# Kernel tuning notes

Hardware: AMD Instinct MI355X
Metric: run time of the kernel (lower is better)

Reference implementation:

```python
import jax, jax.numpy as jnp
import numpy as np

EPS = 1e-6
NUM_HEADS = 16

def _ln(x):
    # LayerNorm32, no affine, eps=1e-6, computed in fp32
    x32 = x.astype(jnp.float32)
    mu = jnp.mean(x32, axis=-1, keepdims=True)
    var = jnp.var(x32, axis=-1, keepdims=True)
    return ((x32 - mu) * jax.lax.rsqrt(var + EPS)).astype(x.dtype)

def _mha(q, k, v):
    # q,k,v: [B, L, H, D]
    d = q.shape[-1]
    scale = 1.0 / jnp.sqrt(jnp.asarray(d, q.dtype))
    s = jnp.einsum('bqhd,bkhd->bhqk', q, k) * scale
    p = jax.nn.softmax(s, axis=-1)
    o = jnp.einsum('bhqk,bkhd->bqhd', p, v)
    return o.reshape(o.shape[0], o.shape[1], -1)

def setup_inputs() -> dict:
    key = jax.random.key(0)
    ks = jax.random.split(key, 10)
    B, L, C, Lc, Cc = 4, 2048, 1024, 1024, 1024
    Dff = 4 * C
    s = 0.02
    return {
        'x': jax.random.normal(ks[0], (B, L, C), jnp.float32),
        'context': jax.random.normal(ks[1], (B, Lc, Cc), jnp.float32),
        'w_qkv': jax.random.normal(ks[2], (C, 3 * C), jnp.float32) * s,
        'b_qkv': jnp.zeros((3 * C,), jnp.float32),
        'w_os': jax.random.normal(ks[3], (C, C), jnp.float32) * s,
        'b_os': jnp.zeros((C,), jnp.float32),
        'w_qc': jax.random.normal(ks[4], (C, C), jnp.float32) * s,
        'b_qc': jnp.zeros((C,), jnp.float32),
        'w_kvc': jax.random.normal(ks[5], (Cc, 2 * C), jnp.float32) * s,
        'b_kvc': jnp.zeros((2 * C,), jnp.float32),
        'w_oc': jax.random.normal(ks[6], (C, C), jnp.float32) * s,
        'b_oc': jnp.zeros((C,), jnp.float32),
        'w_fc1': jax.random.normal(ks[7], (C, Dff), jnp.float32) * s,
        'b_fc1': jnp.zeros((Dff,), jnp.float32),
        'w_fc2': jax.random.normal(ks[8], (Dff, C), jnp.float32) * s,
        'b_fc2': jnp.zeros((C,), jnp.float32),
    }

def reference(x, context, w_qkv, b_qkv, w_os, b_os, w_qc, b_qc, w_kvc, b_kvc,
              w_oc, b_oc, w_fc1, b_fc1, w_fc2, b_fc2):
    B, L, C = x.shape
    H = NUM_HEADS
    D = C // H
    # --- self attention (pre-norm, full) ---
    h = _ln(x)
    qkv = (h @ w_qkv + b_qkv).reshape(B, L, 3, H, D)
    q, k, v = qkv[:, :, 0], qkv[:, :, 1], qkv[:, :, 2]
    h = _mha(q, k, v) @ w_os + b_os
    x = x + h
    # --- cross attention ---
    h = _ln(x)
    q = (h @ w_qc + b_qc).reshape(B, L, H, D)
    Lc = context.shape[1]
    kv = (context @ w_kvc + b_kvc).reshape(B, Lc, 2, H, D)
    k, v = kv[:, :, 0], kv[:, :, 1]
    h = _mha(q, k, v) @ w_oc + b_oc
    x = x + h
    # --- sparse FFN (GELU tanh) ---
    h = _ln(x)
    h = jax.nn.gelu(h @ w_fc1 + b_fc1, approximate=True) @ w_fc2 + b_fc2
    return x + h
```

## Files before the change

### kernel.cpp

```cpp
#include <hip/hip_runtime.h>

typedef unsigned short ushort_t;
typedef __attribute__((ext_vector_type(8))) short short8;
typedef __attribute__((ext_vector_type(4))) float f32x4;
typedef __attribute__((ext_vector_type(4))) unsigned short ushort4v;

__device__ inline ushort_t f2bf(float f) {
    union { float f; unsigned u; } v; v.f = f;
    return (ushort_t)((v.u + 0x7FFFu + ((v.u >> 16) & 1u)) >> 16);
}
__device__ inline float bf2f(ushort_t u) {
    union { unsigned u; float f; } v; v.u = ((unsigned)u) << 16;
    return v.f;
}

__device__ inline void gld16(const ushort_t* g, ushort_t* l) {
    __builtin_amdgcn_global_load_lds(
        (const __attribute__((address_space(1))) unsigned int*)g,
        (__attribute__((address_space(3))) unsigned int*)l, 16, 0, 0);
}

__device__ inline int xcd_swz(int id, int nwg) {
    int q = nwg >> 3;
    return (id & 7) * q + (id >> 3);
}

__global__ void w_transpose_bf16(const float* __restrict__ w, ushort_t* __restrict__ out,
                                 int K, int N) {
    __shared__ float t[64][65];
    const int k0 = blockIdx.y * 64, n0 = blockIdx.x * 64;
    const int tid = threadIdx.x;
#pragma unroll
    for (int i = 0; i < 16; i++) {
        int idx = tid + i * 256;
        int r = idx >> 6, c = idx & 63;
        t[r][c] = w[(size_t)(k0 + r) * N + n0 + c];
    }
    __syncthreads();
#pragma unroll
    for (int i = 0; i < 16; i++) {
        int idx = tid + i * 256;
        int nr = idx >> 6, kc = idx & 63;
        out[(size_t)(n0 + nr) * K + k0 + kc] = f2bf(t[kc][nr]);
    }
}

__global__ void v_transpose(const ushort_t* __restrict__ V, int vStride, int rowsPerBatch,
                            ushort_t* __restrict__ Vt, int Lk) {
    __shared__ __align__(16) ushort_t t[64][72];
    const int bh = blockIdx.y, k0 = blockIdx.x * 64;
    const int b = bh >> 4, h = bh & 15;
    const int tid = threadIdx.x;
    const ushort_t* src = V + (size_t)(b * rowsPerBatch + k0) * vStride + h * 64;
#pragma unroll
    for (int i = 0; i < 2; i++) {
        int ch = tid + i * 256;
        int r = ch >> 3, c = (ch & 7) * 8;
        *(short8*)(&t[r][c]) = *(const short8*)(src + (size_t)r * vStride + c);
    }
    __syncthreads();
#pragma unroll
    for (int i = 0; i < 2; i++) {
        int ch = tid + i * 256;
        int d = ch >> 3, c = (ch & 7) * 8;
        short8 o;
#pragma unroll
        for (int j = 0; j < 8; j++) o[j] = (short)t[c + j][d];
        *(short8*)(Vt + ((size_t)bh * 64 + d) * Lk + k0 + c) = o;
    }
}

__global__ void f32_to_bf16_vec(const float* __restrict__ in, ushort_t* __restrict__ out, int n4) {
    int i = blockIdx.x * blockDim.x + threadIdx.x;
    if (i < n4) {
        float4 v = ((const float4*)in)[i];
        ushort4v o;
        o[0] = f2bf(v.x); o[1] = f2bf(v.y); o[2] = f2bf(v.z); o[3] = f2bf(v.w);
        ((ushort4v*)out)[i] = o;
    }
}

__global__ void ln_rows(const float* __restrict__ in, ushort_t* __restrict__ out) {
    __shared__ float s1[4], s2[4];
    const int row = blockIdx.x;
    const int tid = threadIdx.x;
    const float4 v = ((const float4*)(in + (size_t)row * 1024))[tid];
    float s  = v.x + v.y + v.z + v.w;
    float ss = v.x * v.x + v.y * v.y + v.z * v.z + v.w * v.w;
#pragma unroll
    for (int d = 32; d >= 1; d >>= 1) {
        s  += __shfl_down(s, d, 64);
        ss += __shfl_down(ss, d, 64);
    }
    if ((tid & 63) == 0) { s1[tid >> 6] = s; s2[tid >> 6] = ss; }
    __syncthreads();
    float sum = s1[0] + s1[1] + s1[2] + s1[3];
    float sqs = s2[0] + s2[1] + s2[2] + s2[3];
    float mu  = sum * (1.0f / 1024.0f);
    float var = sqs * (1.0f / 1024.0f) - mu * mu;
    float rs  = rsqrtf(var + 1e-6f);
    ushort4v o;
    o[0] = f2bf((v.x - mu) * rs);
    o[1] = f2bf((v.y - mu) * rs);
    o[2] = f2bf((v.z - mu) * rs);
    o[3] = f2bf((v.w - mu) * rs);
    ((ushort4v*)(out + (size_t)row * 1024))[tid] = o;
}

#define EPI_BF16 0
#define EPI_GELU 1
#define EPI_RES  2

template <int EPI>
__global__ void gemm_bt(const ushort_t* __restrict__ A, const ushort_t* __restrict__ Bt,
                        const float* __restrict__ bias, const float* __restrict__ res,
                        void* __restrict__ outp, int M, int N, int K) {
    __shared__ __align__(16) ushort_t As[128 * 64];
    __shared__ __align__(16) ushort_t Bs[128 * 64];
    const int tid = threadIdx.x;
    const int lane = tid & 63, wave = tid >> 6;
    const int nwg = gridDim.x * gridDim.y;
    const int sid = xcd_swz(blockIdx.y * gridDim.x + blockIdx.x, nwg);
    const int m0 = (sid / gridDim.x) * 128, n0 = (sid % gridDim.x) * 128;
    const int wr = (wave >> 1) * 64, wc = (wave & 1) * 64;
    const int lr = lane & 15, lg = lane >> 4;

    f32x4 acc[4][4];
#pragma unroll
    for (int i = 0; i < 4; i++)
#pragma unroll
        for (int j = 0; j < 4; j++) acc[i][j] = f32x4{0.f, 0.f, 0.f, 0.f};

    for (int k0 = 0; k0 < K; k0 += 64) {
#pragma unroll
        for (int i = 0; i < 4; i++) {
            int ch = tid + i * 256;
            int r = ch >> 3;
            int kcs = (((ch & 7) ^ (r & 7))) * 8;
            gld16(A  + (size_t)(m0 + r) * K + k0 + kcs, As + ch * 8);
            gld16(Bt + (size_t)(n0 + r) * K + k0 + kcs, Bs + ch * 8);
        }
        __syncthreads();
#pragma unroll
        for (int ks = 0; ks < 2; ks++) {
            short8 af[4], bfr[4];
#pragma unroll
            for (int m = 0; m < 4; m++) {
                int r = wr + m * 16 + lr;
                int kc = ks * 4 + lg;
                af[m] = *(const short8*)(As + r * 64 + ((kc ^ (r & 7)) << 3));
            }
#pragma unroll
            for (int n = 0; n < 4; n++) {
                int r = wc + n * 16 + lr;
                int kc = ks * 4 + lg;
                bfr[n] = *(const short8*)(Bs + r * 64 + ((kc ^ (r & 7)) << 3));
            }
#pragma unroll
            for (int m = 0; m < 4; m++)
#pragma unroll
                for (int n = 0; n < 4; n++)
                    acc[m][n] = __builtin_amdgcn_mfma_f32_16x16x32_bf16(af[m], bfr[n], acc[m][n], 0, 0, 0);
        }
        __syncthreads();
    }

#pragma unroll
    for (int m = 0; m < 4; m++) {
        int rowb = m0 + wr + m * 16 + lg * 4;
#pragma unroll
        for (int n = 0; n < 4; n++) {
            int col = n0 + wc + n * 16 + lr;
            float bcol = bias[col];
            f32x4 v = acc[m][n];
#pragma unroll
            for (int q = 0; q < 4; q++) {
                float x = v[q] + bcol;
                if (EPI == EPI_GELU) {
                    float u = 0.7978845608028654f * (x + 0.044715f * x * x * x);
                    x = 0.5f * x * (1.0f + tanhf(u));
                }
                size_t off = (size_t)(rowb + q) * N + col;
                if (EPI == EPI_RES) ((float*)outp)[off] = x + res[off];
                else                ((ushort_t*)outp)[off] = f2bf(x);
            }
        }
    }
}

__global__ __launch_bounds__(512, 2)
void attn_fwd(const ushort_t* __restrict__ Q, int qStride,
              const ushort_t* __restrict__ Kp, int kvStride, int kvBatchRows,
              const ushort_t* __restrict__ Vt, int Lk,
              ushort_t* __restrict__ O) {
    __shared__ __align__(16) ushort_t Ks[2][64 * 64];
    __shared__ __align__(16) ushort_t Vts[2][64 * 64];
    __shared__ __align__(16) ushort_t Ps[8][16 * 64];
    const int tid = threadIdx.x, lane = tid & 63, wave = tid >> 6;
    const int lr = lane & 15, lg = lane >> 4;
    const int sid = xcd_swz(blockIdx.x, gridDim.x);
    const int qb = sid & 15, h = (sid >> 4) & 15, b = sid >> 8;
    const int qRow0 = b * 2048 + qb * 128;
    const int kvRow0 = b * kvBatchRows;
    const int hc = h * 64;
    const ushort_t* vt_base = Vt + (size_t)(b * 16 + h) * 64 * Lk;

    short8 qf[2];
    {
        const ushort_t* qrow = Q + (size_t)(qRow0 + wave * 16 + lr) * qStride + hc;
        short8 r0 = *(const short8*)(qrow + lg * 8);
        short8 r1 = *(const short8*)(qrow + 32 + lg * 8);
#pragma unroll
        for (int j = 0; j < 8; j++) {
            qf[0][j] = (short)f2bf(bf2f((ushort_t)r0[j]) * 0.125f);
            qf[1][j] = (short)f2bf(bf2f((ushort_t)r1[j]) * 0.125f);
        }
    }

    f32x4 oacc[4];
#pragma unroll
    for (int d = 0; d < 4; d++) oacc[d] = f32x4{0.f, 0.f, 0.f, 0.f};
    float mrun = -INFINITY, lrun = 0.f;

    const int nt = Lk >> 6;

    auto stage = [&](int buf, int kt) {
        int r = tid >> 3;
        int kcs = (((tid & 7) ^ (r & 7))) * 8;
        gld16(Kp + (size_t)(kvRow0 + kt + r) * kvStride + hc + kcs, Ks[buf] + tid * 8);
        gld16(vt_base + (size_t)r * Lk + kt + kcs, Vts[buf] + tid * 8);
    };

    stage(0, 0);
    __syncthreads();
    int cur = 0;

    for (int t = 0; t < nt; ++t) {
        if (t + 1 < nt) stage(cur ^ 1, (t + 1) * 64);

        const ushort_t* Kc = Ks[cur];
        const ushort_t* Vc = Vts[cur];

        f32x4 sacc[4];
        __builtin_amdgcn_s_setprio(1);
#pragma unroll
        for (int n = 0; n < 4; n++) {
            int r = n * 16 + lr;
            short8 k0 = *(const short8*)(Kc + r * 64 + ((lg ^ (r & 7)) << 3));
            short8 k1 = *(const short8*)(Kc + r * 64 + (((4 + lg) ^ (r & 7)) << 3));
            f32x4 s = f32x4{0.f, 0.f, 0.f, 0.f};
            s = __builtin_amdgcn_mfma_f32_16x16x32_bf16(k0, qf[0], s, 0, 0, 0);
            s = __builtin_amdgcn_mfma_f32_16x16x32_bf16(k1, qf[1], s, 0, 0, 0);
            sacc[n] = s;
        }
        __builtin_amdgcn_s_setprio(0);

        float mx = sacc[0][0];
#pragma unroll
        for (int n = 0; n < 4; n++)
#pragma unroll
            for (int r = 0; r < 4; r++) if (n | r) mx = fmaxf(mx, sacc[n][r]);
        mx = fmaxf(mx, __shfl_xor(mx, 16, 64));
        mx = fmaxf(mx, __shfl_xor(mx, 32, 64));

        if (!__all(mx <= mrun + 8.0f)) {
            float mnew = fmaxf(mrun, mx);
            float al = __expf(mrun - mnew);
            float a0 = __shfl(al, lg * 4 + 0, 64);
            float a1 = __shfl(al, lg * 4 + 1, 64);
            float a2 = __shfl(al, lg * 4 + 2, 64);
            float a3 = __shfl(al, lg * 4 + 3, 64);
#pragma unroll
            for (int dn = 0; dn < 4; dn++) {
                oacc[dn][0] *= a0; oacc[dn][1] *= a1;
                oacc[dn][2] *= a2; oacc[dn][3] *= a3;
            }
            lrun *= al;
            mrun = mnew;
        }

        float rsum = 0.f;
#pragma unroll
        for (int n = 0; n < 4; n++)
#pragma unroll
            for (int r = 0; r < 4; r++) {
                float p = __expf(sacc[n][r] - mrun);
                sacc[n][r] = p;
                rsum += p;
            }
        rsum += __shfl_xor(rsum, 16, 64);
        rsum += __shfl_xor(rsum, 32, 64);
        lrun += rsum;

        ushort_t* Pw = &Ps[wave][0];
#pragma unroll
        for (int n = 0; n < 4; n++) {
            unsigned w0, w1;
            asm("v_cvt_pk_bf16_f32 %0, %1, %2" : "=v"(w0) : "v"(sacc[n][0]), "v"(sacc[n][1]));
            asm("v_cvt_pk_bf16_f32 %0, %1, %2" : "=v"(w1) : "v"(sacc[n][2]), "v"(sacc[n][3]));
            int kc = n * 2 + (lg >> 1);
            uint2 u; u.x = w0; u.y = w1;
            *(uint2*)((char*)Pw + lr * 128 + ((kc ^ (lr & 7)) << 4) + (lg & 1) * 8) = u;
        }

        short8 pf0 = *(const short8*)(Pw + lr * 64 + ((lg ^ (lr & 7)) << 3));
        short8 pf1 = *(const short8*)(Pw + lr * 64 + (((4 + lg) ^ (lr & 7)) << 3));
        __builtin_amdgcn_s_setprio(1);
#pragma unroll
        for (int dn = 0; dn < 4; dn++) {
            int r = dn * 16 + lr;
            short8 v0 = *(const short8*)(Vc + r * 64 + ((lg ^ (r & 7)) << 3));
            short8 v1 = *(const short8*)(Vc + r * 64 + (((4 + lg) ^ (r & 7)) << 3));
            oacc[dn] = __builtin_amdgcn_mfma_f32_16x16x32_bf16(pf0, v0, oacc[dn], 0, 0, 0);
            oacc[dn] = __builtin_amdgcn_mfma_f32_16x16x32_bf16(pf1, v1, oacc[dn], 0, 0, 0);
        }
        __builtin_amdgcn_s_setprio(0);
        __syncthreads();
        cur ^= 1;
    }

    float linv[4];
#pragma unroll
    for (int r = 0; r < 4; r++) linv[r] = 1.0f / __shfl(lrun, lg * 4 + r, 64);

#pragma unroll
    for (int dn = 0; dn < 4; dn++)
#pragma unroll
        for (int q = 0; q < 4; q++) {
            float o = oacc[dn][q] * linv[q];
            int row = qRow0 + wave * 16 + lg * 4 + q;
            int col = hc + dn * 16 + lr;
            O[(size_t)row * 1024 + col] = f2bf(o);
        }
}

extern "C" void kernel_launch(void* const* d_in, const int* in_sizes, int n_in,
                              void* d_out, int out_size, void* d_ws, size_t ws_size,
                              hipStream_t stream) {
    const float* x     = (const float*)d_in[0];
    const float* ctx   = (const float*)d_in[1];
    const float* w_qkv = (const float*)d_in[2];
    const float* b_qkv = (const float*)d_in[3];
    const float* w_os  = (const float*)d_in[4];
    const float* b_os  = (const float*)d_in[5];
    const float* w_qc  = (const float*)d_in[6];
    const float* b_qc  = (const float*)d_in[7];
    const float* w_kvc = (const float*)d_in[8];
    const float* b_kvc = (const float*)d_in[9];
    const float* w_oc  = (const float*)d_in[10];
    const float* b_oc  = (const float*)d_in[11];
    const float* w_fc1 = (const float*)d_in[12];
    const float* b_fc1 = (const float*)d_in[13];
    const float* w_fc2 = (const float*)d_in[14];
    const float* b_fc2 = (const float*)d_in[15];
    float* out = (float*)d_out;

    char* ws = (char*)d_ws;
    ushort_t* wqkvT = (ushort_t*)(ws + 0);
    ushort_t* wosT  = (ushort_t*)(ws + 6291456);
    ushort_t* wqcT  = (ushort_t*)(ws + 8388608);
    ushort_t* wkvcT = (ushort_t*)(ws + 10485760);
    ushort_t* wocT  = (ushort_t*)(ws + 14680064);
    ushort_t* wfc1T = (ushort_t*)(ws + 16777216);
    ushort_t* wfc2T = (ushort_t*)(ws + 25165824);
    ushort_t* qkv_bf  = (ushort_t*)(ws + 33554432);
    ushort_t* q_bf    = (ushort_t*)(ws + 33554432);
    ushort_t* kv_bf   = (ushort_t*)(ws + 50331648);
    ushort_t* vt_c    = (ushort_t*)(ws + 67108864);
    ushort_t* ffn_bf  = (ushort_t*)(ws + 33554432);
    ushort_t* ctx_bf  = (ushort_t*)(ws + 83886080);
    ushort_t* attn_bf = (ushort_t*)(ws + 92274688);
    ushort_t* h_bf    = (ushort_t*)(ws + 109051904);
    ushort_t* vt_s    = (ushort_t*)(ws + 109051904);

    const dim3 tb(256);
    const dim3 tb512(512);
    w_transpose_bf16<<<dim3(48, 16), tb, 0, stream>>>(w_qkv, wqkvT, 1024, 3072);
    w_transpose_bf16<<<dim3(16, 16), tb, 0, stream>>>(w_os,  wosT,  1024, 1024);
    w_transpose_bf16<<<dim3(16, 16), tb, 0, stream>>>(w_qc,  wqcT,  1024, 1024);
    w_transpose_bf16<<<dim3(32, 16), tb, 0, stream>>>(w_kvc, wkvcT, 1024, 2048);
    w_transpose_bf16<<<dim3(16, 16), tb, 0, stream>>>(w_oc,  wocT,  1024, 1024);
    w_transpose_bf16<<<dim3(64, 16), tb, 0, stream>>>(w_fc1, wfc1T, 1024, 4096);
    w_transpose_bf16<<<dim3(16, 64), tb, 0, stream>>>(w_fc2, wfc2T, 4096, 1024);
    f32_to_bf16_vec<<<4096, tb, 0, stream>>>(ctx, ctx_bf, 1048576);

    ln_rows<<<8192, tb, 0, stream>>>(x, h_bf);
    gemm_bt<EPI_BF16><<<dim3(24, 64), tb, 0, stream>>>(h_bf, wqkvT, b_qkv, nullptr, qkv_bf, 8192, 3072, 1024);
    v_transpose<<<dim3(32, 64), tb, 0, stream>>>(qkv_bf + 2048, 3072, 2048, vt_s, 2048);
    attn_fwd<<<dim3(1024), tb512, 0, stream>>>(qkv_bf, 3072, qkv_bf + 1024, 3072, 2048,
                                               vt_s, 2048, attn_bf);
    gemm_bt<EPI_RES><<<dim3(8, 64), tb, 0, stream>>>(attn_bf, wosT, b_os, x, out, 8192, 1024, 1024);

    ln_rows<<<8192, tb, 0, stream>>>(out, h_bf);
    gemm_bt<EPI_BF16><<<dim3(8, 64), tb, 0, stream>>>(h_bf, wqcT, b_qc, nullptr, q_bf, 8192, 1024, 1024);
    gemm_bt<EPI_BF16><<<dim3(16, 32), tb, 0, stream>>>(ctx_bf, wkvcT, b_kvc, nullptr, kv_bf, 4096, 2048, 1024);
    v_transpose<<<dim3(16, 64), tb, 0, stream>>>(kv_bf + 1024, 2048, 1024, vt_c, 1024);
    attn_fwd<<<dim3(1024), tb512, 0, stream>>>(q_bf, 1024, kv_bf, 2048, 1024,
                                               vt_c, 1024, attn_bf);
    gemm_bt<EPI_RES><<<dim3(8, 64), tb, 0, stream>>>(attn_bf, wocT, b_oc, out, out, 8192, 1024, 1024);

    ln_rows<<<8192, tb, 0, stream>>>(out, h_bf);
    gemm_bt<EPI_GELU><<<dim3(32, 64), tb, 0, stream>>>(h_bf, wfc1T, b_fc1, nullptr, ffn_bf, 8192, 4096, 1024);
    gemm_bt<EPI_RES><<<dim3(8, 64), tb, 0, stream>>>(ffn_bf, wfc2T, b_fc2, out, out, 8192, 1024, 4096);
}
```

Before: 589.6 us.

## Batch weight transposes into one launch, use exp2 softmax and fast tanh

The seven weight-transpose launches become a single kernel that works out which matrix each block handles from a tile-offset table, which cuts launch overhead. Attention folds log2(e) into the Q scale so that exp2f replaces __expf, scales the lazy-rescale threshold to match, and reduces the row max as a tree. The GELU epilogue computes tanh from exp2 instead of calling tanhf. Together these trim launch cost and instruction count in the softmax and GELU paths, with small rounding differences as the trade-off.

```diff
diff --git a/kernel.cpp b/kernel.cpp
--- a/kernel.cpp
+++ b/kernel.cpp
@@ -25,10 +25,25 @@
     return (id & 7) * q + (id >> 3);
 }
 
-__global__ void w_transpose_bf16(const float* __restrict__ w, ushort_t* __restrict__ out,
-                                 int K, int N) {
+struct WPrep {
+    const float* src[7];
+    ushort_t*    dst[7];
+    int K[7], N[7];
+    int tilesBefore[8];
+};
+
+__global__ void w_prep_all(WPrep P) {
     __shared__ float t[64][65];
-    const int k0 = blockIdx.y * 64, n0 = blockIdx.x * 64;
+    const int bid = blockIdx.x;
+    int e = 0;
+#pragma unroll
+    for (int i = 0; i < 7; i++) if (bid >= P.tilesBefore[i + 1]) e = i + 1;
+    const int lt = bid - P.tilesBefore[e];
+    const int K = P.K[e], N = P.N[e];
+    const int ntx = N >> 6;
+    const int n0 = (lt % ntx) * 64, k0 = (lt / ntx) * 64;
+    const float* w = P.src[e];
+    ushort_t* out = P.dst[e];
     const int tid = threadIdx.x;
 #pragma unroll
     for (int i = 0; i < 16; i++) {
@@ -178,7 +193,10 @@
                 float x = v[q] + bcol;
                 if (EPI == EPI_GELU) {
                     float u = 0.7978845608028654f * (x + 0.044715f * x * x * x);
-                    x = 0.5f * x * (1.0f + tanhf(u));
+                    float a = fabsf(u);
+                    float tt = exp2f(-2.885390081777927f * a);
+                    float th = copysignf((1.0f - tt) / (1.0f + tt), u);
+                    x = 0.5f * x * (1.0f + th);
                 }
                 size_t off = (size_t)(rowb + q) * N + col;
                 if (EPI == EPI_RES) ((float*)outp)[off] = x + res[off];
@@ -210,17 +228,18 @@
         const ushort_t* qrow = Q + (size_t)(qRow0 + wave * 16 + lr) * qStride + hc;
         short8 r0 = *(const short8*)(qrow + lg * 8);
         short8 r1 = *(const short8*)(qrow + 32 + lg * 8);
+        const float s = 0.125f * 1.4426950408889634f;
 #pragma unroll
         for (int j = 0; j < 8; j++) {
-            qf[0][j] = (short)f2bf(bf2f((ushort_t)r0[j]) * 0.125f);
-            qf[1][j] = (short)f2bf(bf2f((ushort_t)r1[j]) * 0.125f);
+            qf[0][j] = (short)f2bf(bf2f((ushort_t)r0[j]) * s);
+            qf[1][j] = (short)f2bf(bf2f((ushort_t)r1[j]) * s);
         }
     }
 
     f32x4 oacc[4];
 #pragma unroll
     for (int d = 0; d < 4; d++) oacc[d] = f32x4{0.f, 0.f, 0.f, 0.f};
-    float mrun = -INFINITY, lrun = 0.f;
+    float mrun = -1e30f, lrun = 0.f;
 
     const int nt = Lk >> 6;
 
@@ -255,17 +274,19 @@
         }
         __builtin_amdgcn_s_setprio(0);
 
-        float mx = sacc[0][0];
-#pragma unroll
-        for (int n = 0; n < 4; n++)
-#pragma unroll
-            for (int r = 0; r < 4; r++) if (n | r) mx = fmaxf(mx, sacc[n][r]);
+        float m0 = fmaxf(fmaxf(sacc[0][0], sacc[0][1]), sacc[0][2]);
+        float m1 = fmaxf(fmaxf(sacc[0][3], sacc[1][0]), sacc[1][1]);
+        float m2 = fmaxf(fmaxf(sacc[1][2], sacc[1][3]), sacc[2][0]);
+        float m3 = fmaxf(fmaxf(sacc[2][1], sacc[2][2]), sacc[2][3]);
+        float m4 = fmaxf(fmaxf(sacc[3][0], sacc[3][1]), sacc[3][2]);
+        float mx = fmaxf(fmaxf(fmaxf(m0, m1), fmaxf(m2, m3)),
+                         fmaxf(m4, sacc[3][3]));
         mx = fmaxf(mx, __shfl_xor(mx, 16, 64));
         mx = fmaxf(mx, __shfl_xor(mx, 32, 64));
 
-        if (!__all(mx <= mrun + 8.0f)) {
+        if (!__all(mx <= mrun + 11.5416f)) {
             float mnew = fmaxf(mrun, mx);
-            float al = __expf(mrun - mnew);
+            float al = exp2f(mrun - mnew);
             float a0 = __shfl(al, lg * 4 + 0, 64);
             float a1 = __shfl(al, lg * 4 + 1, 64);
             float a2 = __shfl(al, lg * 4 + 2, 64);
@@ -284,7 +305,7 @@
         for (int n = 0; n < 4; n++)
 #pragma unroll
             for (int r = 0; r < 4; r++) {
-                float p = __expf(sacc[n][r] - mrun);
+                float p = exp2f(sacc[n][r] - mrun);
                 sacc[n][r] = p;
                 rsum += p;
             }
@@ -375,13 +396,19 @@
 
     const dim3 tb(256);
     const dim3 tb512(512);
-    w_transpose_bf16<<<dim3(48, 16), tb, 0, stream>>>(w_qkv, wqkvT, 1024, 3072);
-    w_transpose_bf16<<<dim3(16, 16), tb, 0, stream>>>(w_os,  wosT,  1024, 1024);
-    w_transpose_bf16<<<dim3(16, 16), tb, 0, stream>>>(w_qc,  wqcT,  1024, 1024);
-    w_transpose_bf16<<<dim3(32, 16), tb, 0, stream>>>(w_kvc, wkvcT, 1024, 2048);
-    w_transpose_bf16<<<dim3(16, 16), tb, 0, stream>>>(w_oc,  wocT,  1024, 1024);
-    w_transpose_bf16<<<dim3(64, 16), tb, 0, stream>>>(w_fc1, wfc1T, 1024, 4096);
-    w_transpose_bf16<<<dim3(16, 64), tb, 0, stream>>>(w_fc2, wfc2T, 4096, 1024);
+
+    WPrep P;
+    P.src[0] = w_qkv; P.dst[0] = wqkvT; P.K[0] = 1024; P.N[0] = 3072;
+    P.src[1] = w_os;  P.dst[1] = wosT;  P.K[1] = 1024; P.N[1] = 1024;
+    P.src[2] = w_qc;  P.dst[2] = wqcT;  P.K[2] = 1024; P.N[2] = 1024;
+    P.src[3] = w_kvc; P.dst[3] = wkvcT; P.K[3] = 1024; P.N[3] = 2048;
+    P.src[4] = w_oc;  P.dst[4] = wocT;  P.K[4] = 1024; P.N[4] = 1024;
+    P.src[5] = w_fc1; P.dst[5] = wfc1T; P.K[5] = 1024; P.N[5] = 4096;
+    P.src[6] = w_fc2; P.dst[6] = wfc2T; P.K[6] = 4096; P.N[6] = 1024;
+    P.tilesBefore[0] = 0;
+    for (int i = 0; i < 7; i++)
+        P.tilesBefore[i + 1] = P.tilesBefore[i] + (P.N[i] / 64) * (P.K[i] / 64);
+    w_prep_all<<<dim3(P.tilesBefore[7]), tb, 0, stream>>>(P);
     f32_to_bf16_vec<<<4096, tb, 0, stream>>>(ctx, ctx_bf, 1048576);
 
     ln_rows<<<8192, tb, 0, stream>>>(x, h_bf);
```

Result: slower. 606.1 us (+2.8%).
